# Performance work log

Measured on AMD Instinct MI355X. Metric: run time of the kernel, lower is better.

The kernel has to match this reference:

```python
import jax, jax.numpy as jnp
import numpy as np
from jax import lax

T = 256        # sentence length
V = 50000      # vocab
NT = 50        # POS tags
NL = 40        # dependency labels
WD, TD = 300, 100
IN = WD + TD   # 400, LSTM input & hidden size
H = IN
BI = 2 * H     # 800, biLSTM output per token
MI = 2 * BI    # 1600, MLP input/hidden size


def setup_inputs() -> dict:
    key = jax.random.key(0)
    ks = jax.random.split(key, 32)
    s = 0.05
    d = {
        'words': jax.random.randint(ks[0], (T,), 0, V),
        'tags': jax.random.randint(ks[1], (T,), 0, NT),
        'arcs': jax.random.randint(ks[2], (T + 1,), 0, T + 1),
        'h0': jax.random.normal(ks[3], (4, 1, H), jnp.float32),
        'c0': jax.random.normal(ks[4], (4, 1, H), jnp.float32),
        'word_emb': jax.random.normal(ks[5], (V, WD), jnp.float32) * s,
        'tag_emb': jax.random.normal(ks[6], (NT, TD), jnp.float32) * s,
        # LSTM layer 0: input IN; layer 1: input BI. Leading dim 2 = directions (fwd, rev).
        'Wih0': jax.random.normal(ks[7], (2, 4 * H, IN), jnp.float32) * s,
        'Whh0': jax.random.normal(ks[8], (2, 4 * H, H), jnp.float32) * s,
        'bih0': jax.random.normal(ks[9], (2, 4 * H), jnp.float32) * s,
        'bhh0': jax.random.normal(ks[10], (2, 4 * H), jnp.float32) * s,
        'Wih1': jax.random.normal(ks[11], (2, 4 * H, BI), jnp.float32) * s,
        'Whh1': jax.random.normal(ks[12], (2, 4 * H, H), jnp.float32) * s,
        'bih1': jax.random.normal(ks[13], (2, 4 * H), jnp.float32) * s,
        'bhh1': jax.random.normal(ks[14], (2, 4 * H), jnp.float32) * s,
        # arc-score MLP: 1600 -> 1600 -> 1 (Linear, Tanh, Linear)
        'Wa1': jax.random.normal(ks[15], (MI, MI), jnp.float32) * s,
        'ba1': jax.random.normal(ks[16], (MI,), jnp.float32) * s,
        'Wa2': jax.random.normal(ks[17], (1, MI), jnp.float32) * s,
        'ba2': jax.random.normal(ks[18], (1,), jnp.float32) * s,
        # label MLP: 1600 -> 1600 -> 40
        'Wl1': jax.random.normal(ks[19], (MI, MI), jnp.float32) * s,
        'bl1': jax.random.normal(ks[20], (MI,), jnp.float32) * s,
        'Wl2': jax.random.normal(ks[21], (NL, MI), jnp.float32) * s,
        'bl2': jax.random.normal(ks[22], (NL,), jnp.float32) * s,
    }
    return d


def _lstm_dir(x, Wih, Whh, bih, bhh, h, c):
    # x: [T, in]; returns [T, H]. Torch gate order i, f, g, o.
    xg = x @ Wih.T + (bih + bhh)  # precompute input projection: [T, 4H]

    def step(carry, xt):
        h, c = carry
        g = xt + h @ Whh.T
        i, f, gg, o = jnp.split(g, 4, axis=-1)
        i, f, o = jax.nn.sigmoid(i), jax.nn.sigmoid(f), jax.nn.sigmoid(o)
        c = f * c + i * jnp.tanh(gg)
        h = o * jnp.tanh(c)
        return (h, c), h

    (_, _), ys = lax.scan(step, (h, c), xg)
    return ys


def _bilstm_layer(x, Wih, Whh, bih, bhh, h0f, c0f, h0b, c0b):
    fwd = _lstm_dir(x, Wih[0], Whh[0], bih[0], bhh[0], h0f, c0f)
    bwd = _lstm_dir(x[::-1], Wih[1], Whh[1], bih[1], bhh[1], h0b, c0b)[::-1]
    return jnp.concatenate([fwd, bwd], axis=-1)


def _mlp(z, W1, b1, W2, b2):
    return jnp.tanh(z @ W1.T + b1) @ W2.T + b2


def reference(words, tags, arcs, h0, c0, word_emb, tag_emb,
              Wih0, Whh0, bih0, bhh0, Wih1, Whh1, bih1, bhh1,
              Wa1, ba1, Wa2, ba2, Wl1, bl1, Wl2, bl2):
    n = words.shape[0]
    x = jnp.concatenate([word_emb[words], tag_emb[tags]], axis=-1)  # [T, 400]
    x1 = _bilstm_layer(x, Wih0, Whh0, bih0, bhh0, h0[0, 0], c0[0, 0], h0[1, 0], c0[1, 0])
    hV = _bilstm_layer(x1, Wih1, Whh1, bih1, bhh1, h0[2, 0], c0[2, 0], h0[3, 0], c0[3, 0])  # [T, 800]

    # All-pairs arc scores: feats[h, d] = concat(hV[h], hV[d]) -> MLP -> scalar.
    hh = jnp.broadcast_to(hV[:, None, :], (n, n, BI))
    dd = jnp.broadcast_to(hV[None, :, :], (n, n, BI))
    feats = jnp.concatenate([hh, dd], axis=-1)  # [T, T, 1600]
    raw = _mlp(feats, Wa1, ba1, Wa2, ba2)[..., 0]  # [T, T]
    raw = raw * (1.0 - jnp.eye(n, dtype=raw.dtype))  # head == dep left at 0
    scores = jnp.zeros((n + 1, n + 1), raw.dtype).at[1:, 1:].set(raw).at[0, 0].set(1.0)

    # Labels: for token i with gold head h (1-based), concat(hV[i], hV[h-1]); head==0 -> zeros.
    heads = arcs[1:]
    idx = jnp.clip(heads - 1, 0, n - 1)
    lf = jnp.concatenate([hV, hV[idx]], axis=-1)  # [T, 1600]
    lab = _mlp(lf, Wl1, bl1, Wl2, bl2)  # [T, 40]
    lab = jnp.where((heads == 0)[:, None], jnp.zeros_like(lab), lab)
    return (scores, lab)
```

## Files before the change

### kernel.cpp

```cpp
#include <hip/hip_runtime.h>

typedef unsigned int   u32;
typedef unsigned long long u64;

__device__ __forceinline__ float fast_tanh(float x) {
    x = fminf(fmaxf(x, -15.f), 15.f);
    float e = __expf(2.f * x);
    return __fdividef(e - 1.f, e + 1.f);
}

#define HLD(p) __hip_atomic_load((p), __ATOMIC_RELAXED, __HIP_MEMORY_SCOPE_AGENT)

#define OF_XG   ((size_t)0)
#define OF_H    (OF_XG + 3276800)
#define OF_PQ   (OF_H  + 1638400)
#define OF_U    (OF_PQ + 3276800)

struct H4 { u64 v0, v1, v2, v3; const u64* p; u32 want; };

__device__ __forceinline__ H4 h4_issue(const u64* __restrict__ hist, int t, int k, u32 base) {
    H4 h;
    if (k < 400) { h.p = hist + (size_t)t * 400 + k;                          h.want = base + (u32)t + 1u; }
    else         { h.p = hist + 102400 + (size_t)(255 - t) * 400 + (k - 400); h.want = base + (u32)(255 - t) + 1u; }
    h.v0 = HLD(h.p + 0); h.v1 = HLD(h.p + 1); h.v2 = HLD(h.p + 2); h.v3 = HLD(h.p + 3);
    return h;
}

__device__ __forceinline__ float4 h4_fin(H4 h) {
    while ((u32)(h.v0 >> 32) != h.want || (u32)(h.v1 >> 32) != h.want ||
           (u32)(h.v2 >> 32) != h.want || (u32)(h.v3 >> 32) != h.want) {
        __builtin_amdgcn_s_sleep(4);
        h.v0 = HLD(h.p + 0); h.v1 = HLD(h.p + 1); h.v2 = HLD(h.p + 2); h.v3 = HLD(h.p + 3);
    }
    return make_float4(__uint_as_float((u32)h.v0), __uint_as_float((u32)h.v1),
                       __uint_as_float((u32)h.v2), __uint_as_float((u32)h.v3));
}

__device__ __forceinline__ void gate_wait(const u64* __restrict__ w0, const u64* __restrict__ w1,
                                          u32 want0, u32 want1) {
    if (threadIdx.x == 0) {
        for (;;) {
            u32 g0 = (u32)(HLD(w0) >> 32);
            u32 g1 = (u32)(HLD(w1) >> 32);
            if (g0 == want0 && g1 == want1) break;
            __builtin_amdgcn_s_sleep(16);
        }
    }
    __syncthreads();
}

__device__ __forceinline__ void stage_nb(float (*As)[68], float (*Bs)[68],
                                         int lk, int lr, float4 av, float4 bv) {
    As[lk + 0][lr] = av.x; As[lk + 1][lr] = av.y; As[lk + 2][lr] = av.z; As[lk + 3][lr] = av.w;
    Bs[lk + 0][lr] = bv.x; Bs[lk + 1][lr] = bv.y; Bs[lk + 2][lr] = bv.z; Bs[lk + 3][lr] = bv.w;
}

__device__ __forceinline__ void fma16(float acc[4][4], const float (*As)[68], const float (*Bs)[68],
                                      int tx, int ty) {
    #pragma unroll
    for (int kk = 0; kk < 16; ++kk) {
        float4 a4 = *(const float4*)&As[kk][ty * 4];
        float4 b4 = *(const float4*)&Bs[kk][tx * 4];
        acc[0][0] += a4.x * b4.x; acc[0][1] += a4.x * b4.y; acc[0][2] += a4.x * b4.z; acc[0][3] += a4.x * b4.w;
        acc[1][0] += a4.y * b4.x; acc[1][1] += a4.y * b4.y; acc[1][2] += a4.y * b4.z; acc[1][3] += a4.y * b4.w;
        acc[2][0] += a4.z * b4.x; acc[2][1] += a4.z * b4.y; acc[2][2] += a4.z * b4.z; acc[2][3] += a4.z * b4.w;
        acc[3][0] += a4.w * b4.x; acc[3][1] += a4.w * b4.y; acc[3][2] += a4.w * b4.z; acc[3][3] += a4.w * b4.w;
    }
}

__device__ __forceinline__ void gemm_seg(float (*AsB)[16][68], float (*BsB)[16][68],
        float acc[4][4], const u64* __restrict__ hist, int t, int tind, u32 base,
        const float* __restrict__ brow, int kb, int klen,
        int lk, int lr, int tx, int ty, int& pb)
{
    int ka = kb + lk;
    H4 h = h4_issue(hist, ka < 800 ? t : tind, ka < 800 ? ka : ka - 800, base);
    float4 bv = *(const float4*)(brow + ka);
    for (int k0 = kb; k0 < kb + klen; k0 += 16) {
        float4 av = h4_fin(h);
        stage_nb(AsB[pb], BsB[pb], lk, lr, av, bv);
        int kn = k0 + 16;
        if (kn < kb + klen) {
            int k2 = kn + lk;
            h  = h4_issue(hist, k2 < 800 ? t : tind, k2 < 800 ? k2 : k2 - 800, base);
            bv = *(const float4*)(brow + k2);
        }
        __syncthreads();
        fma16(acc, AsB[pb], BsB[pb], tx, ty);
        pb ^= 1;
    }
}

__global__ __launch_bounds__(256)
void gemm_embed_kernel(const int* __restrict__ words, const int* __restrict__ tags,
                       const float* __restrict__ wemb, const float* __restrict__ temb,
                       const float* __restrict__ B,
                       const float* __restrict__ bias1, const float* __restrict__ bias2,
                       float* __restrict__ C) {
    int t0 = blockIdx.x * 64;
    int n0 = blockIdx.y * 64;
    int tid = threadIdx.x;
    int tx = tid & 15, ty = tid >> 4;
    int lr = tid >> 2, lk = (tid & 3) * 4;
    __shared__ float As[2][16][68];
    __shared__ float Bs[2][16][68];
    float acc[4][4] = {};

    int t = t0 + lr;
    const float* arow0 = wemb + (size_t)words[t] * 300;
    const float* arow1 = temb + (size_t)tags[t] * 100 - 300;
    const float* brow  = B + (size_t)(n0 + lr) * 400;

    int p = 0;
    float4 av, bv;
    { int k = lk; av = (k < 300) ? *(const float4*)(arow0 + k) : *(const float4*)(arow1 + k);
      bv = *(const float4*)(brow + k); }
    for (int k0 = 0; k0 < 400; k0 += 16) {
        stage_nb(As[p], Bs[p], lk, lr, av, bv);
        int kn = k0 + 16;
        if (kn < 400) {
            int k = kn + lk;
            av = (k < 300) ? *(const float4*)(arow0 + k) : *(const float4*)(arow1 + k);
            bv = *(const float4*)(brow + k);
        }
        __syncthreads();
        fma16(acc, As[p], Bs[p], tx, ty);
        p ^= 1;
    }
    float bs[4];
    #pragma unroll
    for (int j = 0; j < 4; ++j) {
        int n = n0 + tx * 4 + j;
        bs[j] = bias1[n] + bias2[n];
    }
    #pragma unroll
    for (int i = 0; i < 4; ++i) {
        int tr = t0 + ty * 4 + i;
        float4 o;
        o.x = acc[i][0] + bs[0]; o.y = acc[i][1] + bs[1];
        o.z = acc[i][2] + bs[2]; o.w = acc[i][3] + bs[3];
        *(float4*)(C + (size_t)tr * 3200 + n0 + tx * 4) = o;
    }
}

#define LSTM_G 50
__device__ __forceinline__ void lstm_body(int bid,
                 const float* __restrict__ Whh,
                 const float* __restrict__ h0,
                 const float* __restrict__ c0,
                 int hc_base,
                 const float* __restrict__ xg,
                 u64* __restrict__ hist,
                 u32 tag_base,
                 float (*hbuf)[416]) {
    const int T = 256;
    int d  = bid / LSTM_G;
    int wg = bid % LSTM_G;
    int a8 = wg * 8;
    int tid = threadIdx.x;
    int w = tid >> 6, lane = tid & 63;
    int c = lane & 7, r = lane >> 3;
    int gate = r >> 1, jj = r & 1;
    int gr = gate * 400 + a8 + 2 * w + jj;

    float4 wv[13];
    const float* wrow = Whh + (size_t)d * 640000 + (size_t)gr * 400;
    #pragma unroll
    for (int i = 0; i < 13; ++i) {
        int k = 4 * (c + 8 * i);
        wv[i] = (k + 3 < 400) ? *(const float4*)(wrow + k) : make_float4(0.f, 0.f, 0.f, 0.f);
    }
    if (tid < 16) { hbuf[0][400 + tid] = 0.f; hbuf[1][400 + tid] = 0.f; }

    float c_state = 0.f;
    if (lane == 0 || lane == 8)
        c_state = c0[(hc_base + d) * 400 + a8 + 2 * w + jj];

    u64* hst = hist + (size_t)d * 102400;
    bool need2 = (tid + 256 < 400);

    for (int t = 0; t < T; ++t) {
        int xt = d ? (T - 1 - t) : t;
        float xgv = xg[(size_t)xt * 3200 + d * 1600 + gr];
        float* hb = hbuf[t & 1];

        if (t == 0) {
            hb[tid] = h0[(hc_base + d) * 400 + tid];
            if (need2) hb[tid + 256] = h0[(hc_base + d) * 400 + tid + 256];
        } else {
            const u64* src = hst + (size_t)(t - 1) * 400;
            u32 want = tag_base + (u32)t;
            bool d1 = false, d2 = !need2;
            while (!(d1 && d2)) {
                u64 v1 = 0, v2 = 0;
                if (!d1) v1 = HLD(&src[tid]);
                if (!d2) v2 = HLD(&src[tid + 256]);
                if (!d1 && (u32)(v1 >> 32) == want) { hb[tid] = __uint_as_float((u32)v1); d1 = true; }
                if (!d2 && (u32)(v2 >> 32) == want) { hb[tid + 256] = __uint_as_float((u32)v2); d2 = true; }
            }
        }
        __syncthreads();

        const float4* h4 = (const float4*)hb;
        float s = 0.f;
        #pragma unroll
        for (int i = 0; i < 13; ++i) {
            float4 hv = h4[c + 8 * i];
            s += wv[i].x * hv.x + wv[i].y * hv.y + wv[i].z * hv.z + wv[i].w * hv.w;
        }
        s += __shfl_down(s, 4);
        s += __shfl_down(s, 2);
        s += __shfl_down(s, 1);

        float v = 0.f;
        if (c == 0) {
            float tot = s + xgv;
            float arg = (gate == 2) ? 2.f * tot : -tot;
            arg = fminf(fmaxf(arg, -60.f), 60.f);
            float e = __expf(arg);
            v = (gate == 2) ? (e - 1.f) * __frcp_rn(e + 1.f)
                            : __frcp_rn(1.f + e);
        }
        float fv = __shfl(v, lane + 16);
        float gv = __shfl(v, lane + 32);
        float ov = __shfl(v, lane + 48);
        if (lane == 0 || lane == 8) {
            c_state = fv * c_state + v * gv;
            float ec = __expf(fminf(fmaxf(2.f * c_state, -60.f), 60.f));
            float th = (ec - 1.f) * __frcp_rn(ec + 1.f);
            float h = ov * th;
            u64 pk = (((u64)(tag_base + t + 1)) << 32) | (u64)__float_as_uint(h);
            __hip_atomic_store(&hst[(size_t)t * 400 + a8 + 2 * w + jj], pk,
                               __ATOMIC_RELAXED, __HIP_MEMORY_SCOPE_AGENT);
        }
    }
}

union SmemU {
    struct { float As[2][16][68]; float Bs[2][16][68]; } g;
    float hbuf[2][416];
};

__global__ __launch_bounds__(256)
void lstm0_fused(const float* __restrict__ Whh, const float* __restrict__ h0,
                 const float* __restrict__ c0, const float* __restrict__ xg0,
                 u64* __restrict__ hist,
                 const float* __restrict__ Wih1, const float* __restrict__ bih1,
                 const float* __restrict__ bhh1, float* __restrict__ xg1) {
    __shared__ SmemU sm;
    int bid = blockIdx.x;
    if (bid < 2 * LSTM_G) {
        lstm_body(bid, Whh, h0, c0, 0, xg0, hist, 0u, sm.hbuf);
        return;
    }
    int g = bid - 2 * LSTM_G;
    int t0 = (g & 3) * 64;
    int n0 = (g >> 2) * 64;
    int tid = threadIdx.x;
    int tx = tid & 15, ty = tid >> 4;
    int lr = tid >> 2, lk = (tid & 3) * 4;
    float acc[4][4] = {};
    int t = t0 + lr;
    const float* brow = Wih1 + (size_t)(n0 + lr) * 800;

    int first = (t0 >= 128) ? 400 : 0;
    int pb = 0;
    for (int seg = 0; seg < 2; ++seg) {
        int kb = first ^ (seg ? 400 : 0);
        if (kb == 0) {
            const u64* gw = hist + (size_t)(t0 + 63) * 400;
            gate_wait(gw, gw + 399, (u32)(t0 + 64), (u32)(t0 + 64));
        } else {
            const u64* gw = hist + 102400 + (size_t)(255 - t0) * 400;
            gate_wait(gw, gw + 399, (u32)(256 - t0), (u32)(256 - t0));
        }
        gemm_seg(sm.g.As, sm.g.Bs, acc, hist, t, t, 0u, brow, kb, 400, lk, lr, tx, ty, pb);
    }
    float bs[4];
    #pragma unroll
    for (int j = 0; j < 4; ++j) {
        int n = n0 + tx * 4 + j;
        bs[j] = bih1[n] + bhh1[n];
    }
    #pragma unroll
    for (int i = 0; i < 4; ++i) {
        int tr = t0 + ty * 4 + i;
        float4 o;
        o.x = acc[i][0] + bs[0]; o.y = acc[i][1] + bs[1];
        o.z = acc[i][2] + bs[2]; o.w = acc[i][3] + bs[3];
        *(float4*)(xg1 + (size_t)tr * 3200 + n0 + tx * 4) = o;
    }
}

__global__ __launch_bounds__(256)
void lstm1_fused(const float* __restrict__ Whh, const float* __restrict__ h0,
                 const float* __restrict__ c0, const float* __restrict__ xg1,
                 u64* __restrict__ hist, const int* __restrict__ arcs,
                 const float* __restrict__ Wa1, const float* __restrict__ ba1,
                 const float* __restrict__ Wl1, const float* __restrict__ bl1,
                 float* __restrict__ PQ, float* __restrict__ U) {
    __shared__ SmemU sm;
    int bid = blockIdx.x;
    if (bid < 2 * LSTM_G) {
        lstm_body(bid, Whh, h0, c0, 2, xg1, hist, 256u, sm.hbuf);
        return;
    }
    int g = bid - 2 * LSTM_G;
    int t0 = (g & 3) * 64;
    int by = g >> 2;
    int tid = threadIdx.x;
    int tx = tid & 15, ty = tid >> 4;
    int lr = tid >> 2, lk = (tid & 3) * 4;
    float acc[4][4] = {};
    int t = t0 + lr;
    int first = (t0 >= 128) ? 400 : 0;
    int pb = 0;

    if (by < 25) {
        int n0 = by * 64;
        int h = arcs[1 + t];
        int tind = min(max(h - 1, 0), 255);
        const float* brow = Wl1 + (size_t)(n0 + lr) * 1600;
        for (int seg = 0; seg < 3; ++seg) {
            int kb   = (seg < 2) ? (first ^ (seg ? 400 : 0)) : 800;
            int klen = (seg < 2) ? 400 : 800;
            if (seg < 2) {
                if (kb == 0) {
                    const u64* gw = hist + (size_t)(t0 + 63) * 400;
                    gate_wait(gw, gw + 399, (u32)(t0 + 320), (u32)(t0 + 320));
                } else {
                    const u64* gw = hist + 102400 + (size_t)(255 - t0) * 400;
                    gate_wait(gw, gw + 399, (u32)(512 - t0), (u32)(512 - t0));
                }
            } else {
                const u64* gf = hist + (size_t)255 * 400;
                const u64* gb = hist + 102400 + (size_t)255 * 400;
                gate_wait(gf, gb, 512u, 512u);
            }
            gemm_seg(sm.g.As, sm.g.Bs, acc, hist, t, tind, 256u, brow, kb, klen, lk, lr, tx, ty, pb);
        }
        float bs[4];
        #pragma unroll
        for (int j = 0; j < 4; ++j) bs[j] = bl1[n0 + tx * 4 + j];
        #pragma unroll
        for (int i = 0; i < 4; ++i) {
            int tr = t0 + ty * 4 + i;
            float4 o;
            o.x = fast_tanh(acc[i][0] + bs[0]); o.y = fast_tanh(acc[i][1] + bs[1]);
            o.z = fast_tanh(acc[i][2] + bs[2]); o.w = fast_tanh(acc[i][3] + bs[3]);
            *(float4*)(U + (size_t)tr * 1600 + n0 + tx * 4) = o;
        }
    } else {
        int n0 = (by - 25) * 64;
        int nn = n0 + lr;
        const float* brow = (nn < 1600) ? Wa1 + (size_t)nn * 1600
                                        : Wa1 + (size_t)(nn - 1600) * 1600 + 800;
        for (int seg = 0; seg < 2; ++seg) {
            int kb = first ^ (seg ? 400 : 0);
            if (kb == 0) {
                const u64* gw = hist + (size_t)(t0 + 63) * 400;
                gate_wait(gw, gw + 399, (u32)(t0 + 320), (u32)(t0 + 320));
            } else {
                const u64* gw = hist + 102400 + (size_t)(255 - t0) * 400;
                gate_wait(gw, gw + 399, (u32)(512 - t0), (u32)(512 - t0));
            }
            gemm_seg(sm.g.As, sm.g.Bs, acc, hist, t, t, 256u, brow, kb, 400, lk, lr, tx, ty, pb);
        }
        float bs[4];
        #pragma unroll
        for (int j = 0; j < 4; ++j) {
            int n = n0 + tx * 4 + j;
            bs[j] = (n < 1600) ? ba1[n] : 0.f;
        }
        #pragma unroll
        for (int i = 0; i < 4; ++i) {
            int tr = t0 + ty * 4 + i;
            float4 o;
            o.x = acc[i][0] + bs[0]; o.y = acc[i][1] + bs[1];
            o.z = acc[i][2] + bs[2]; o.w = acc[i][3] + bs[3];
            *(float4*)(PQ + (size_t)tr * 3200 + n0 + tx * 4) = o;
        }
    }
}

__global__ __launch_bounds__(256)
void arc_kernel(const float* __restrict__ PQ,
                const float* __restrict__ Wa2, const float* __restrict__ ba2,
                float* __restrict__ out) {
    int i0 = blockIdx.x * 16, j0 = blockIdx.y * 16;
    int tid = threadIdx.x;
    int ii = tid >> 4, jj = tid & 15;
    __shared__ float Pt[16][65], Qt[16][65];
    __shared__ float W2f[1600];

    if (i0 == 0 && j0 == 0) {
        if (tid < 257) out[tid] = (tid == 0) ? 1.0f : 0.0f;
        out[(size_t)(tid + 1) * 257] = 0.0f;
        if (tid == 0) out[0] = 1.0f;
    }
    for (int m = tid; m < 1600; m += 256) W2f[m] = Wa2[m];
    __syncthreads();

    float acc = 0.f;
    int mm = tid & 63, r4 = tid >> 6;
    for (int m0 = 0; m0 < 1600; m0 += 64) {
        #pragma unroll
        for (int rr = r4; rr < 16; rr += 4) {
            Pt[rr][mm] = PQ[(size_t)(i0 + rr) * 3200 + m0 + mm];
            Qt[rr][mm] = PQ[(size_t)(j0 + rr) * 3200 + 1600 + m0 + mm];
        }
        __syncthreads();
        #pragma unroll 8
        for (int m = 0; m < 64; ++m) {
            float s = Pt[ii][m] + Qt[jj][m];
            acc += W2f[m0 + m] * fast_tanh(s);
        }
        __syncthreads();
    }
    float raw = acc + ba2[0];
    int gi = i0 + ii, gj = j0 + jj;
    if (gi == gj) raw = 0.f;
    out[(size_t)(gi + 1) * 257 + (gj + 1)] = raw;
}

__global__ __launch_bounds__(256)
void label_out_kernel(const float* __restrict__ U, const float* __restrict__ Wl2,
                      const float* __restrict__ bl2, const int* __restrict__ arcs,
                      float* __restrict__ out) {
    int t = blockIdx.x;
    __shared__ float u_l[1600];
    __shared__ float part[4][64];
    for (int m = threadIdx.x; m < 1600; m += 256) u_l[m] = U[(size_t)t * 1600 + m];
    __syncthreads();
    int tid = threadIdx.x;
    int n = tid & 63, p = tid >> 6;
    float acc = 0.f;
    if (n < 40) {
        const float4* wr4 = (const float4*)(Wl2 + (size_t)n * 1600 + p * 400);
        const float*  ub  = u_l + p * 400;
        for (int m = 0; m < 100; ++m) {
            float4 w = wr4[m];
            acc += ub[4*m] * w.x + ub[4*m+1] * w.y + ub[4*m+2] * w.z + ub[4*m+3] * w.w;
        }
    }
    part[p][n] = acc;
    __syncthreads();
    if (tid < 40) {
        float v = part[0][tid] + part[1][tid] + part[2][tid] + part[3][tid] + bl2[tid];
        if (arcs[1 + t] == 0) v = 0.f;
        out[(size_t)t * 40 + tid] = v;
    }
}

extern "C" void kernel_launch(void* const* d_in, const int* in_sizes, int n_in,
                              void* d_out, int out_size, void* d_ws, size_t ws_size,
                              hipStream_t stream) {
    const int*   words = (const int*)d_in[0];
    const int*   tags  = (const int*)d_in[1];
    const int*   arcs  = (const int*)d_in[2];
    const float* h0    = (const float*)d_in[3];
    const float* c0    = (const float*)d_in[4];
    const float* wemb  = (const float*)d_in[5];
    const float* temb  = (const float*)d_in[6];
    const float* Wih0  = (const float*)d_in[7];
    const float* Whh0  = (const float*)d_in[8];
    const float* bih0  = (const float*)d_in[9];
    const float* bhh0  = (const float*)d_in[10];
    const float* Wih1  = (const float*)d_in[11];
    const float* Whh1  = (const float*)d_in[12];
    const float* bih1  = (const float*)d_in[13];
    const float* bhh1  = (const float*)d_in[14];
    const float* Wa1   = (const float*)d_in[15];
    const float* ba1   = (const float*)d_in[16];
    const float* Wa2   = (const float*)d_in[17];
    const float* ba2   = (const float*)d_in[18];
    const float* Wl1   = (const float*)d_in[19];
    const float* bl1   = (const float*)d_in[20];
    const float* Wl2   = (const float*)d_in[21];
    const float* bl2   = (const float*)d_in[22];
    float* out = (float*)d_out;

    char* ws = (char*)d_ws;
    float* xg0  = (float*)(ws + OF_XG);
    u64*   hist = (u64*)  (ws + OF_H);
    float* xg1  = (float*)(ws + OF_PQ);
    float* PQ   = (float*)(ws + OF_XG);
    float* U    = (float*)(ws + OF_U);

    gemm_embed_kernel<<<dim3(4, 50), 256, 0, stream>>>(words, tags, wemb, temb, Wih0, bih0, bhh0, xg0);
    lstm0_fused<<<300, 256, 0, stream>>>(Whh0, h0, c0, xg0, hist, Wih1, bih1, bhh1, xg1);
    lstm1_fused<<<400, 256, 0, stream>>>(Whh1, h0, c0, xg1, hist, arcs, Wa1, ba1, Wl1, bl1, PQ, U);
    arc_kernel<<<dim3(16, 16), 256, 0, stream>>>(PQ, Wa2, ba2, out);
    label_out_kernel<<<256, 256, 0, stream>>>(U, Wl2, bl2, arcs, out + 66049);
}
```

Measured before the change: 1.139 ms.

## Merge both LSTM layers into one kernel with counter gating; retile arc kernel

Folds the layer-0 LSTM, the layer-1 input GEMM, the layer-1 LSTM and the MLP first-layer GEMMs into a single 700-block kernel. The stages are ordered by global atomic counters instead of kernel boundaries, which removes one launch and lets layer-1 blocks load their weights while layer 0 still runs. The counters live in a scratch slot of the output buffer that the arc kernel later overwrites. The arc kernel switches to 8x8 tiles with a four-way split over the hidden dimension and a shared-memory reduction, giving four times more blocks. The design relies on all 700 blocks being co-resident so the spin waits cannot deadlock.

```diff
diff --git a/kernel.cpp b/kernel.cpp
--- a/kernel.cpp
+++ b/kernel.cpp
@@ -45,6 +45,15 @@
             if (g0 == want0 && g1 == want1) break;
             __builtin_amdgcn_s_sleep(16);
         }
+    }
+    __syncthreads();
+}
+
+__device__ __forceinline__ void gate_cnt(const u32* __restrict__ c, u32 target) {
+    if (threadIdx.x == 0) {
+        while (__hip_atomic_load(c, __ATOMIC_RELAXED, __HIP_MEMORY_SCOPE_AGENT) < target)
+            __builtin_amdgcn_s_sleep(16);
+        (void)__hip_atomic_load(c, __ATOMIC_ACQUIRE, __HIP_MEMORY_SCOPE_AGENT);
     }
     __syncthreads();
 }
@@ -96,10 +105,11 @@
                        const float* __restrict__ wemb, const float* __restrict__ temb,
                        const float* __restrict__ B,
                        const float* __restrict__ bias1, const float* __restrict__ bias2,
-                       float* __restrict__ C) {
+                       float* __restrict__ C, u32* __restrict__ cnt) {
     int t0 = blockIdx.x * 64;
     int n0 = blockIdx.y * 64;
     int tid = threadIdx.x;
+    if (blockIdx.x == 0 && blockIdx.y == 0 && tid < 4) cnt[tid] = 0u;
     int tx = tid & 15, ty = tid >> 4;
     int lr = tid >> 2, lk = (tid & 3) * 4;
     __shared__ float As[2][16][68];
@@ -152,7 +162,8 @@
                  const float* __restrict__ xg,
                  u64* __restrict__ hist,
                  u32 tag_base,
-                 float (*hbuf)[416]) {
+                 float (*hbuf)[416],
+                 const u32* __restrict__ cnt) {
     const int T = 256;
     int d  = bid / LSTM_G;
     int wg = bid % LSTM_G;
@@ -175,6 +186,8 @@
     float c_state = 0.f;
     if (lane == 0 || lane == 8)
         c_state = c0[(hc_base + d) * 400 + a8 + 2 * w + jj];
+
+    if (cnt) { gate_cnt(&cnt[0], 50); gate_cnt(&cnt[1], 50); gate_cnt(&cnt[2], 50); gate_cnt(&cnt[3], 50); }
 
     u64* hst = hist + (size_t)d * 102400;
     bool need2 = (tid + 256 < 400);
@@ -242,82 +255,83 @@
 };
 
 __global__ __launch_bounds__(256)
-void lstm0_fused(const float* __restrict__ Whh, const float* __restrict__ h0,
-                 const float* __restrict__ c0, const float* __restrict__ xg0,
-                 u64* __restrict__ hist,
+void mega_kernel(const float* __restrict__ Whh0, const float* __restrict__ Whh1,
+                 const float* __restrict__ h0, const float* __restrict__ c0,
+                 const float* __restrict__ xg0, float* __restrict__ xg1,
+                 u64* __restrict__ hist, const int* __restrict__ arcs,
                  const float* __restrict__ Wih1, const float* __restrict__ bih1,
-                 const float* __restrict__ bhh1, float* __restrict__ xg1) {
+                 const float* __restrict__ bhh1,
+                 const float* __restrict__ Wa1, const float* __restrict__ ba1,
+                 const float* __restrict__ Wl1, const float* __restrict__ bl1,
+                 float* __restrict__ PQ, float* __restrict__ U, u32* __restrict__ cnt) {
     __shared__ SmemU sm;
     int bid = blockIdx.x;
-    if (bid < 2 * LSTM_G) {
-        lstm_body(bid, Whh, h0, c0, 0, xg0, hist, 0u, sm.hbuf);
+    int tid = threadIdx.x;
+
+    if (bid < 100) {
+        lstm_body(bid, Whh0, h0, c0, 0, xg0, hist, 0u, sm.hbuf, nullptr);
         return;
     }
-    int g = bid - 2 * LSTM_G;
-    int t0 = (g & 3) * 64;
-    int n0 = (g >> 2) * 64;
-    int tid = threadIdx.x;
+    if (bid < 300) {
+        int g = bid - 100;
+        int t0 = (g & 3) * 64;
+        int n0 = (g >> 2) * 64;
+        int tx = tid & 15, ty = tid >> 4;
+        int lr = tid >> 2, lk = (tid & 3) * 4;
+        float acc[4][4] = {};
+        int t = t0 + lr;
+        const float* brow = Wih1 + (size_t)(n0 + lr) * 800;
+
+        int first = (t0 >= 128) ? 400 : 0;
+        int pb = 0;
+        for (int seg = 0; seg < 2; ++seg) {
+            int kb = first ^ (seg ? 400 : 0);
+            if (kb == 0) {
+                const u64* gw = hist + (size_t)(t0 + 63) * 400;
+                gate_wait(gw, gw + 399, (u32)(t0 + 64), (u32)(t0 + 64));
+            } else {
+                const u64* gw = hist + 102400 + (size_t)(255 - t0) * 400;
+                gate_wait(gw, gw + 399, (u32)(256 - t0), (u32)(256 - t0));
+            }
+            gemm_seg(sm.g.As, sm.g.Bs, acc, hist, t, t, 0u, brow, kb, 400, lk, lr, tx, ty, pb);
+        }
+        float bs[4];
+        #pragma unroll
+        for (int j = 0; j < 4; ++j) {
+            int n = n0 + tx * 4 + j;
+            bs[j] = bih1[n] + bhh1[n];
+        }
+        #pragma unroll
+        for (int i = 0; i < 4; ++i) {
+            int tr = t0 + ty * 4 + i;
+            float4 o;
+            o.x = acc[i][0] + bs[0]; o.y = acc[i][1] + bs[1];
+            o.z = acc[i][2] + bs[2]; o.w = acc[i][3] + bs[3];
+            *(float4*)(xg1 + (size_t)tr * 3200 + n0 + tx * 4) = o;
+        }
+        __syncthreads();
+        if (tid == 0)
+            __hip_atomic_fetch_add(&cnt[t0 >> 6], 1u, __ATOMIC_RELEASE, __HIP_MEMORY_SCOPE_AGENT);
+        return;
+    }
+    if (bid < 400) {
+        lstm_body(bid - 300, Whh1, h0, c0, 2, xg1, hist, 256u, sm.hbuf, cnt);
+        return;
+    }
+
+    gate_cnt(&cnt[0], 50); gate_cnt(&cnt[1], 50); gate_cnt(&cnt[2], 50); gate_cnt(&cnt[3], 50);
+
     int tx = tid & 15, ty = tid >> 4;
     int lr = tid >> 2, lk = (tid & 3) * 4;
     float acc[4][4] = {};
-    int t = t0 + lr;
-    const float* brow = Wih1 + (size_t)(n0 + lr) * 800;
-
-    int first = (t0 >= 128) ? 400 : 0;
     int pb = 0;
-    for (int seg = 0; seg < 2; ++seg) {
-        int kb = first ^ (seg ? 400 : 0);
-        if (kb == 0) {
-            const u64* gw = hist + (size_t)(t0 + 63) * 400;
-            gate_wait(gw, gw + 399, (u32)(t0 + 64), (u32)(t0 + 64));
-        } else {
-            const u64* gw = hist + 102400 + (size_t)(255 - t0) * 400;
-            gate_wait(gw, gw + 399, (u32)(256 - t0), (u32)(256 - t0));
-        }
-        gemm_seg(sm.g.As, sm.g.Bs, acc, hist, t, t, 0u, brow, kb, 400, lk, lr, tx, ty, pb);
-    }
-    float bs[4];
-    #pragma unroll
-    for (int j = 0; j < 4; ++j) {
-        int n = n0 + tx * 4 + j;
-        bs[j] = bih1[n] + bhh1[n];
-    }
-    #pragma unroll
-    for (int i = 0; i < 4; ++i) {
-        int tr = t0 + ty * 4 + i;
-        float4 o;
-        o.x = acc[i][0] + bs[0]; o.y = acc[i][1] + bs[1];
-        o.z = acc[i][2] + bs[2]; o.w = acc[i][3] + bs[3];
-        *(float4*)(xg1 + (size_t)tr * 3200 + n0 + tx * 4) = o;
-    }
-}
-
-__global__ __launch_bounds__(256)
-void lstm1_fused(const float* __restrict__ Whh, const float* __restrict__ h0,
-                 const float* __restrict__ c0, const float* __restrict__ xg1,
-                 u64* __restrict__ hist, const int* __restrict__ arcs,
-                 const float* __restrict__ Wa1, const float* __restrict__ ba1,
-                 const float* __restrict__ Wl1, const float* __restrict__ bl1,
-                 float* __restrict__ PQ, float* __restrict__ U) {
-    __shared__ SmemU sm;
-    int bid = blockIdx.x;
-    if (bid < 2 * LSTM_G) {
-        lstm_body(bid, Whh, h0, c0, 2, xg1, hist, 256u, sm.hbuf);
-        return;
-    }
-    int g = bid - 2 * LSTM_G;
-    int t0 = (g & 3) * 64;
-    int by = g >> 2;
-    int tid = threadIdx.x;
-    int tx = tid & 15, ty = tid >> 4;
-    int lr = tid >> 2, lk = (tid & 3) * 4;
-    float acc[4][4] = {};
-    int t = t0 + lr;
-    int first = (t0 >= 128) ? 400 : 0;
-    int pb = 0;
-
-    if (by < 25) {
-        int n0 = by * 64;
+
+    if (bid < 500) {
+        int g = bid - 400;
+        int t0 = (g & 3) * 64;
+        int n0 = (g >> 2) * 64;
+        int t = t0 + lr;
+        int first = (t0 >= 128) ? 400 : 0;
         int h = arcs[1 + t];
         int tind = min(max(h - 1, 0), 255);
         const float* brow = Wl1 + (size_t)(n0 + lr) * 1600;
@@ -351,7 +365,11 @@
             *(float4*)(U + (size_t)tr * 1600 + n0 + tx * 4) = o;
         }
     } else {
-        int n0 = (by - 25) * 64;
+        int g = bid - 500;
+        int t0 = (g & 3) * 64;
+        int n0 = (g >> 2) * 64;
+        int t = t0 + lr;
+        int first = (t0 >= 128) ? 400 : 0;
         int nn = n0 + lr;
         const float* brow = (nn < 1600) ? Wa1 + (size_t)nn * 1600
                                         : Wa1 + (size_t)(nn - 1600) * 1600 + 800;
@@ -387,40 +405,44 @@
 void arc_kernel(const float* __restrict__ PQ,
                 const float* __restrict__ Wa2, const float* __restrict__ ba2,
                 float* __restrict__ out) {
-    int i0 = blockIdx.x * 16, j0 = blockIdx.y * 16;
+    int i0 = blockIdx.x * 8, j0 = blockIdx.y * 8;
     int tid = threadIdx.x;
-    int ii = tid >> 4, jj = tid & 15;
-    __shared__ float Pt[16][65], Qt[16][65];
+    __shared__ float Pt[8][66], Qt[8][66];
     __shared__ float W2f[1600];
-
-    if (i0 == 0 && j0 == 0) {
+    __shared__ float part[4][64];
+
+    if (blockIdx.x == 0 && blockIdx.y == 0) {
         if (tid < 257) out[tid] = (tid == 0) ? 1.0f : 0.0f;
         out[(size_t)(tid + 1) * 257] = 0.0f;
         if (tid == 0) out[0] = 1.0f;
     }
     for (int m = tid; m < 1600; m += 256) W2f[m] = Wa2[m];
-    __syncthreads();
-
+
+    int out_i = tid & 63, ii = out_i >> 3, jj = out_i & 7, mc = tid >> 6;
+    int slr = tid >> 5, slc = (tid & 31) * 2;
     float acc = 0.f;
-    int mm = tid & 63, r4 = tid >> 6;
     for (int m0 = 0; m0 < 1600; m0 += 64) {
-        #pragma unroll
-        for (int rr = r4; rr < 16; rr += 4) {
-            Pt[rr][mm] = PQ[(size_t)(i0 + rr) * 3200 + m0 + mm];
-            Qt[rr][mm] = PQ[(size_t)(j0 + rr) * 3200 + 1600 + m0 + mm];
-        }
+        float2 pv = *(const float2*)(PQ + (size_t)(i0 + slr) * 3200 + m0 + slc);
+        float2 qv = *(const float2*)(PQ + (size_t)(j0 + slr) * 3200 + 1600 + m0 + slc);
         __syncthreads();
-        #pragma unroll 8
-        for (int m = 0; m < 64; ++m) {
+        Pt[slr][slc] = pv.x; Pt[slr][slc + 1] = pv.y;
+        Qt[slr][slc] = qv.x; Qt[slr][slc + 1] = qv.y;
+        __syncthreads();
+        #pragma unroll
+        for (int mm = 0; mm < 16; ++mm) {
+            int m = mc * 16 + mm;
             float s = Pt[ii][m] + Qt[jj][m];
             acc += W2f[m0 + m] * fast_tanh(s);
         }
-        __syncthreads();
-    }
-    float raw = acc + ba2[0];
-    int gi = i0 + ii, gj = j0 + jj;
-    if (gi == gj) raw = 0.f;
-    out[(size_t)(gi + 1) * 257 + (gj + 1)] = raw;
+    }
+    part[mc][out_i] = acc;
+    __syncthreads();
+    if (tid < 64) {
+        float raw = part[0][tid] + part[1][tid] + part[2][tid] + part[3][tid] + ba2[0];
+        int gi = i0 + (tid >> 3), gj = j0 + (tid & 7);
+        if (gi == gj) raw = 0.f;
+        out[(size_t)(gi + 1) * 257 + (gj + 1)] = raw;
+    }
 }
 
 __global__ __launch_bounds__(256)
@@ -486,10 +508,11 @@
     float* xg1  = (float*)(ws + OF_PQ);
     float* PQ   = (float*)(ws + OF_XG);
     float* U    = (float*)(ws + OF_U);
-
-    gemm_embed_kernel<<<dim3(4, 50), 256, 0, stream>>>(words, tags, wemb, temb, Wih0, bih0, bhh0, xg0);
-    lstm0_fused<<<300, 256, 0, stream>>>(Whh0, h0, c0, xg0, hist, Wih1, bih1, bhh1, xg1);
-    lstm1_fused<<<400, 256, 0, stream>>>(Whh1, h0, c0, xg1, hist, arcs, Wa1, ba1, Wl1, bl1, PQ, U);
-    arc_kernel<<<dim3(16, 16), 256, 0, stream>>>(PQ, Wa2, ba2, out);
+    u32*   cnt  = (u32*)out + 66040;
+
+    gemm_embed_kernel<<<dim3(4, 50), 256, 0, stream>>>(words, tags, wemb, temb, Wih0, bih0, bhh0, xg0, cnt);
+    mega_kernel<<<700, 256, 0, stream>>>(Whh0, Whh1, h0, c0, xg0, xg1, hist, arcs,
+                                         Wih1, bih1, bhh1, Wa1, ba1, Wl1, bl1, PQ, U, cnt);
+    arc_kernel<<<dim3(32, 32), 256, 0, stream>>>(PQ, Wa2, ba2, out);
     label_out_kernel<<<256, 256, 0, stream>>>(U, Wl2, bl2, arcs, out + 66049);
 }
```

Measured after the change: 1.137 ms. Within noise of the previous version (-0.1%).
